# Performance work log

Hardware: AMD Instinct MI355X
Metric: run time of the kernel (lower is better)

The kernel has to match this reference:

```python
import jax, jax.numpy as jnp
import numpy as np

N, E = 50000, 800000
INF, ONF, HNF = 64, 64, 128
EPS = 1e-8


def qmul(p, q):
    # roma XYZW Hamilton product
    px, py, pz, pw = p[:, 0], p[:, 1], p[:, 2], p[:, 3]
    qx, qy, qz, qw = q[:, 0], q[:, 1], q[:, 2], q[:, 3]
    return jnp.stack([
        pw * qx + px * qw + py * qz - pz * qy,
        pw * qy - px * qz + py * qw + pz * qx,
        pw * qz + px * qy - py * qx + pz * qw,
        pw * qw - px * qx - py * qy - pz * qz,
    ], axis=1)


def qinv(q):
    conj = jnp.concatenate([-q[:, :3], q[:, 3:]], axis=1)
    return conj / jnp.sum(q * q, axis=1, keepdims=True)


def rot_apply(q, v):
    # rotate v by unit quaternion q (XYZW)
    qv, w = q[:, :3], q[:, 3:4]
    t = 2.0 * jnp.cross(qv, v)
    return v + w * t + jnp.cross(qv, t)


def quat_exponential(im):
    r = jnp.linalg.norm(im, axis=1, keepdims=True)
    u = im / r
    return jnp.concatenate([u * jnp.sin(r), jnp.cos(r)], axis=1)


def seg_sum(data, ids, n):
    return jax.ops.segment_sum(data, ids, num_segments=n)


def seg_mean(data, ids, n):
    s = seg_sum(data, ids, n)
    c = seg_sum(jnp.ones_like(data), ids, n)
    return s / jnp.maximum(c, 1.0)


def setup_inputs() -> dict:
    key = jax.random.key(0)
    ks = jax.random.split(key, 24)
    h = jax.random.normal(ks[0], (N, INF), jnp.float32)
    coord = jax.random.normal(ks[1], (N, 3), jnp.float32)
    q = jax.random.normal(ks[2], (N, 4), jnp.float32)
    quat = q / jnp.linalg.norm(q, axis=1, keepdims=True)
    edge_index = jax.random.randint(ks[3], (2, E), 0, N)

    def lin(k, fi, fo, scale=None):
        s = (1.0 / np.sqrt(fi)) if scale is None else scale
        return jax.random.uniform(k, (fi, fo), jnp.float32, -s, s)

    ein = 2 * INF + 8  # source, target, radial(1), quat_prod(4), unit_vecs(3)
    params = dict(
        We1=lin(ks[4], ein, HNF), be1=jnp.zeros((HNF,), jnp.float32),
        We2=lin(ks[5], HNF, HNF), be2=jnp.zeros((HNF,), jnp.float32),
        Wn1=lin(ks[6], HNF + INF, HNF), bn1=jnp.zeros((HNF,), jnp.float32),
        Wn2=lin(ks[7], HNF, ONF), bn2=jnp.zeros((ONF,), jnp.float32),
        Wc1=lin(ks[8], HNF, HNF), bc1=jnp.zeros((HNF,), jnp.float32),
        wc2=lin(ks[9], HNF, 1, scale=0.001),  # xavier gain 0.001, no bias
        Wq1=lin(ks[10], HNF, HNF), bq1=jnp.zeros((HNF,), jnp.float32),
        Wq2=lin(ks[11], HNF, 3), bq2=jnp.zeros((3,), jnp.float32),
    )
    return dict(h=h, edge_index=edge_index, coord=coord, quat=quat, **params)


def reference(h, edge_index, coord, quat,
              We1, be1, We2, be2, Wn1, bn1, Wn2, bn2,
              Wc1, bc1, wc2, Wq1, bq1, Wq2, bq2):
    silu = jax.nn.silu
    row, col = edge_index[0], edge_index[1]

    # invariants
    coord_diff = coord[row] - coord[col]                       # [E,3]
    qi = qinv(quat)
    quat_prod = qmul(qi[row], quat[col])                       # [E,4]
    radial = jnp.sum(coord_diff ** 2, axis=1, keepdims=True)   # [E,1]
    norm = jnp.sqrt(radial) + EPS
    unit_vecs = -rot_apply(qi[row], coord_diff / norm)         # [E,3]

    # edge model
    ein = jnp.concatenate([h[row], h[col], radial, quat_prod, unit_vecs], axis=1)
    edge_feat = silu(silu(ein @ We1 + be1) @ We2 + be2)        # [E,HNF]

    # coord model (mean agg)
    trans = coord_diff * (silu(edge_feat @ Wc1 + bc1) @ wc2)   # [E,3]
    coord = coord + seg_mean(trans, row, N)

    # quat model (mean agg)
    tan_vecs = silu(edge_feat @ Wq1 + bq1) @ Wq2 + bq2         # [E,3]
    rots = quat_exponential(seg_mean(tan_vecs, row, N))
    quat = qmul(quat, rots)

    # node model (sum agg), residual
    agg = seg_sum(edge_feat, row, N)
    nin = jnp.concatenate([h, agg], axis=1)
    h = h + (silu(nin @ Wn1 + bn1) @ Wn2 + bn2)
    return (h, coord, quat)
```

## Files before the change

### kernel.cpp

```cpp
#include <hip/hip_runtime.h>
#include <hip/hip_bf16.h>
#include <math.h>


#define N_NODES 50000
#define N_EDGES 800000
#define ASTR 172
#define NSTR 204

typedef __attribute__((ext_vector_type(4))) float f32x4;
typedef __attribute__((ext_vector_type(8))) short bf16x8;
typedef __attribute__((ext_vector_type(4))) unsigned short u16x4;
typedef __attribute__((ext_vector_type(8))) unsigned short u16x8;

static __device__ __forceinline__ unsigned short f2bf(float f) {
  return __builtin_bit_cast(unsigned short, __float2bfloat16(f));
}
static __device__ __forceinline__ float bf2f(unsigned short s) {
  unsigned int u = ((unsigned int)s) << 16;
  return __builtin_bit_cast(float, u);
}
static __device__ __forceinline__ float silu_f(float x) {
  return x * __builtin_amdgcn_rcpf(1.0f + __expf(-x));
}
static __device__ __forceinline__ void atomic_pk_add_bf16(unsigned int* addr,
                                                          float lo, float hi) {
  const unsigned int pk = ((unsigned int)f2bf(hi) << 16) | (unsigned int)f2bf(lo);
  asm volatile("global_atomic_pk_add_bf16 %0, %1, off"
               :: "v"((unsigned long long)(uintptr_t)addr), "v"(pk)
               : "memory");
}

static __device__ __forceinline__ void swz_do(const float* __restrict__ src,
                                              unsigned short* __restrict__ dst,
                                              int K, int NOUT, int NCT, int idx) {
  int lane = idx & 63, blk = idx >> 6;
  int ct = blk % NCT, kt = blk / NCT;
  int col = ct * 16 + (lane & 15);
  int kb = kt * 32 + (lane >> 4) * 8;
  u16x8 o;
  #pragma unroll
  for (int j = 0; j < 8; ++j) {
    int k = kb + j;
    o[j] = (k < K) ? f2bf(src[(size_t)k * NOUT + col]) : (unsigned short)0;
  }
  *(u16x8*)(dst + (size_t)idx * 8) = o;
}

__global__ __launch_bounds__(256) void prep1_kernel(
    const float* __restrict__ We1, const float* __restrict__ We2,
    const float* __restrict__ Wc1, const float* __restrict__ Wq1,
    const float* __restrict__ Wn1, const float* __restrict__ Wn2,
    const float* __restrict__ h,
    unsigned short* __restrict__ We1b, unsigned short* __restrict__ We2b,
    unsigned short* __restrict__ Wc1b, unsigned short* __restrict__ Wq1b,
    unsigned short* __restrict__ Wn1b, unsigned short* __restrict__ Wn2b,
    unsigned short* __restrict__ hb, uint4* __restrict__ zbase,
    const int* __restrict__ ei, int* __restrict__ cursor)
{
  const int b = blockIdx.x, t = threadIdx.x;
  if (b < 50) {
    if (b < 10)       swz_do(We1, We1b, 136, 128, 8, b*256 + t);
    else if (b < 18)  swz_do(We2, We2b, 128, 128, 8, (b-10)*256 + t);
    else if (b < 26)  swz_do(Wc1, Wc1b, 128, 128, 8, (b-18)*256 + t);
    else if (b < 34)  swz_do(Wq1, Wq1b, 128, 128, 8, (b-26)*256 + t);
    else if (b < 46) { int i = (b-34)*256 + t; if (i < 3072) swz_do(Wn1, Wn1b, 192, 128, 8, i); }
    else              swz_do(Wn2, Wn2b, 128, 64, 4, (b-46)*256 + t);
    return;
  }
  if (b < 832) {
    const int i16 = (b - 50) * 4096 + t * 16;
    if (i16 < N_NODES * 64) {
      u16x8 o0, o1;
      #pragma unroll
      for (int half = 0; half < 2; ++half) {
        f32x4 v0 = *(const f32x4*)(h + i16 + half*8);
        f32x4 v1 = *(const f32x4*)(h + i16 + half*8 + 4);
        #pragma unroll
        for (int i = 0; i < 4; ++i) {
          if (half == 0) { o0[i] = f2bf(v0[i]); o0[i+4] = f2bf(v1[i]); }
          else           { o1[i] = f2bf(v0[i]); o1[i+4] = f2bf(v1[i]); }
        }
      }
      *(u16x8*)(hb + i16) = o0;
      *(u16x8*)(hb + i16 + 8) = o1;
    }
    return;
  }
  if (b < 1687) {
    const int i = (b - 832) * 256 + t;
    if (i < 218750) {
      uint4 z; z.x = z.y = z.z = z.w = 0u;
      const int base = i * 4;
      zbase[base+0] = z; zbase[base+1] = z; zbase[base+2] = z; zbase[base+3] = z;
    }
    return;
  }
  const int e = (b - 1687) * 256 + t;
  if (e < N_EDGES) atomicAdd(&cursor[ei[e]], 1);
}

__global__ void scan_kernel(int* __restrict__ cursor) {
  __shared__ int s[1024];
  const int t = threadIdx.x;
  const int C = 49;
  const int base = t * C;
  int sum = 0;
  for (int i = 0; i < C; ++i) {
    int n = base + i;
    if (n < N_NODES) sum += cursor[n];
  }
  s[t] = sum;
  __syncthreads();
  for (int d = 1; d < 1024; d <<= 1) {
    int v = (t >= d) ? s[t - d] : 0;
    __syncthreads();
    s[t] += v;
    __syncthreads();
  }
  int run = s[t] - sum;
  for (int i = 0; i < C; ++i) {
    int n = base + i;
    if (n < N_NODES) {
      int d = cursor[n];
      cursor[n] = run;
      run += d;
    }
  }
}

__global__ void scatter_kernel(const int* __restrict__ ei, int* __restrict__ cursor,
                               int2* __restrict__ rc2) {
  int e = blockIdx.x * blockDim.x + threadIdx.x;
  if (e < N_EDGES) {
    int r = ei[e];
    int pos = atomicAdd(&cursor[r], 1);
    int2 v; v.x = r; v.y = ei[N_EDGES + e];
    rc2[pos] = v;
  }
}

template <int KT, int NCT>
static __device__ __forceinline__ void mmW2(const unsigned short* __restrict__ a0,
                                            const unsigned short* __restrict__ a1,
                                            int lk,
                                            const unsigned short* __restrict__ Wb,
                                            const float* __restrict__ bias,
                                            int lane, f32x4* acc0, f32x4* acc1) {
  #pragma unroll
  for (int ct = 0; ct < NCT; ++ct) {
    const f32x4 b = *(const f32x4*)&bias[ct*16 + lk*4];
    acc0[ct] = b; acc1[ct] = b;
  }
  __builtin_amdgcn_s_setprio(1);
  #pragma unroll
  for (int kt = 0; kt < KT; ++kt) {
    bf16x8 x0 = *(const bf16x8*)(a0 + kt*32 + lk*8);
    bf16x8 x1 = *(const bf16x8*)(a1 + kt*32 + lk*8);
    const u16x8* bb = (const u16x8*)Wb + (size_t)(kt*NCT)*64 + lane;
    #pragma unroll
    for (int ct = 0; ct < NCT; ++ct) {
      bf16x8 w = *(const bf16x8*)(bb + (size_t)ct*64);
      acc0[ct] = __builtin_amdgcn_mfma_f32_16x16x32_bf16(w, x0, acc0[ct], 0, 0, 0);
      acc1[ct] = __builtin_amdgcn_mfma_f32_16x16x32_bf16(w, x1, acc1[ct], 0, 0, 0);
    }
  }
  __builtin_amdgcn_s_setprio(0);
}

__global__ __launch_bounds__(128, 3) void edge_kernel(
    const unsigned short* __restrict__ hb,
    const float* __restrict__ coord, const float* __restrict__ quat,
    const int2* __restrict__ rc2,
    const unsigned short* __restrict__ We1b, const unsigned short* __restrict__ We2b,
    const unsigned short* __restrict__ Wc1b, const unsigned short* __restrict__ Wq1b,
    const float* __restrict__ be1, const float* __restrict__ be2,
    const float* __restrict__ bc1, const float* __restrict__ wc2,
    const float* __restrict__ bq1, const float* __restrict__ Wq2,
    const float* __restrict__ bq2,
    unsigned int* __restrict__ agg32, float* __restrict__ transS,
    float* __restrict__ tanS)
{
  __shared__ __align__(16) unsigned short AF[64 * ASTR];

  const int tid = threadIdx.x;
  const int wv = tid >> 6, lane = tid & 63;
  const int lr = lane & 15, lk = lane >> 4;
  const int row0 = wv*32 + lr, row1 = row0 + 16;

  const int xcd = blockIdx.x & 7, idx = blockIdx.x >> 3;
  const int q = 1562, rem = 4;
  const int bid = (xcd < rem ? xcd*(q+1) : rem*(q+1) + (xcd-rem)*q) + idx;
  const int e0 = bid * 64;

  const int2 p0v = rc2[e0 + row0];
  const int2 p1v = rc2[e0 + row1];
  const int r0 = p0v.x, c0 = p0v.y, r1 = p1v.x, c1 = p1v.y;

  {
    const unsigned short* hs0 = hb + (size_t)(lk < 2 ? r0 : c0) * 64 + (lk & 1) * 32;
    const unsigned short* hs1 = hb + (size_t)(lk < 2 ? r1 : c1) * 64 + (lk & 1) * 32;
    const int cb = lk * 32;
    #pragma unroll
    for (int j = 0; j < 32; j += 4) {
      *(u16x4*)&AF[row0*ASTR + cb + j] = *(const u16x4*)(hs0 + j);
      *(u16x4*)&AF[row1*ASTR + cb + j] = *(const u16x4*)(hs1 + j);
    }
  }
  const float cdx0 = coord[r0*3+0] - coord[c0*3+0];
  const float cdy0 = coord[r0*3+1] - coord[c0*3+1];
  const float cdz0 = coord[r0*3+2] - coord[c0*3+2];
  const float cdx1 = coord[r1*3+0] - coord[c1*3+0];
  const float cdy1 = coord[r1*3+1] - coord[c1*3+1];
  const float cdz1 = coord[r1*3+2] - coord[c1*3+2];
  if (lk < 2) {
    const int gr = lk ? r1 : r0, gc = lk ? c1 : c0, grow = lk ? row1 : row0;
    const float gx = lk ? cdx1 : cdx0, gy = lk ? cdy1 : cdy0, gz = lk ? cdz1 : cdz0;
    const float radial = gx*gx + gy*gy + gz*gz;
    const float nrm = sqrtf(radial) + 1e-8f;
    const f32x4 qr4 = *(const f32x4*)&quat[gr*4];
    const f32x4 qc4 = *(const f32x4*)&quat[gc*4];
    const float qix = -qr4[0], qiy = -qr4[1], qiz = -qr4[2], qiw = qr4[3];
    const float qcx = qc4[0], qcy = qc4[1], qcz = qc4[2], qcw = qc4[3];
    const float qpx = qiw*qcx + qix*qcw + qiy*qcz - qiz*qcy;
    const float qpy = qiw*qcy - qix*qcz + qiy*qcw + qiz*qcx;
    const float qpz = qiw*qcz + qix*qcy - qiy*qcx + qiz*qcw;
    const float qpw = qiw*qcw - qix*qcx - qiy*qcy - qiz*qcz;
    const float rinv = __builtin_amdgcn_rcpf(nrm);
    const float vx = gx*rinv, vy = gy*rinv, vz = gz*rinv;
    const float tx = 2.f*(qiy*vz - qiz*vy);
    const float ty = 2.f*(qiz*vx - qix*vz);
    const float tz = 2.f*(qix*vy - qiy*vx);
    const float ux = -(vx + qiw*tx + (qiy*tz - qiz*ty));
    const float uy = -(vy + qiw*ty + (qiz*tx - qix*tz));
    const float uz = -(vz + qiw*tz + (qix*ty - qiy*tx));
    u16x4 f0, f1;
    f0[0] = f2bf(radial); f0[1] = f2bf(qpx); f0[2] = f2bf(qpy); f0[3] = f2bf(qpz);
    f1[0] = f2bf(qpw);    f1[1] = f2bf(ux);  f1[2] = f2bf(uy);  f1[3] = f2bf(uz);
    *(u16x4*)&AF[grow*ASTR + 128] = f0;
    *(u16x4*)&AF[grow*ASTR + 132] = f1;
    const u16x4 z4 = {0, 0, 0, 0};
    #pragma unroll
    for (int j = 136; j < 160; j += 4) *(u16x4*)&AF[grow*ASTR + j] = z4;
  }

  f32x4 acc0[8], acc1[8];

  mmW2<5,8>(AF + row0*ASTR, AF + row1*ASTR, lk, We1b, be1, lane, acc0, acc1);
  #pragma unroll
  for (int ct = 0; ct < 8; ++ct) {
    const int ocb = ct*16 + lk*4;
    u16x4 k0, k1;
    #pragma unroll
    for (int i = 0; i < 4; ++i) {
      k0[i] = f2bf(silu_f(acc0[ct][i]));
      k1[i] = f2bf(silu_f(acc1[ct][i]));
    }
    *(u16x4*)&AF[row0*ASTR + ocb] = k0;
    *(u16x4*)&AF[row1*ASTR + ocb] = k1;
  }

  mmW2<4,8>(AF + row0*ASTR, AF + row1*ASTR, lk, We2b, be2, lane, acc0, acc1);
  #pragma unroll
  for (int ct = 0; ct < 8; ++ct) {
    const int ocb = ct*16 + lk*4;
    u16x4 k0, k1;
    #pragma unroll
    for (int i = 0; i < 4; ++i) {
      k0[i] = f2bf(silu_f(acc0[ct][i]));
      k1[i] = f2bf(silu_f(acc1[ct][i]));
    }
    *(u16x4*)&AF[row0*ASTR + ocb] = k0;
    *(u16x4*)&AF[row1*ASTR + ocb] = k1;
  }

  float pcs0 = 0.f, pcs1 = 0.f;
  mmW2<4,8>(AF + row0*ASTR, AF + row1*ASTR, lk, Wc1b, bc1, lane, acc0, acc1);
  #pragma unroll
  for (int ct = 0; ct < 8; ++ct) {
    const f32x4 w4 = *(const f32x4*)&wc2[ct*16 + lk*4];
    #pragma unroll
    for (int i = 0; i < 4; ++i) {
      pcs0 += silu_f(acc0[ct][i]) * w4[i];
      pcs1 += silu_f(acc1[ct][i]) * w4[i];
    }
  }
  pcs0 += __shfl_xor(pcs0, 16);  pcs0 += __shfl_xor(pcs0, 32);
  pcs1 += __shfl_xor(pcs1, 16);  pcs1 += __shfl_xor(pcs1, 32);

  float p00 = 0.f, p10 = 0.f, p20 = 0.f;
  float p01 = 0.f, p11 = 0.f, p21 = 0.f;
  mmW2<4,8>(AF + row0*ASTR, AF + row1*ASTR, lk, Wq1b, bq1, lane, acc0, acc1);
  #pragma unroll
  for (int ct = 0; ct < 8; ++ct) {
    const float* wq = &Wq2[(ct*16 + lk*4)*3];
    const f32x4 qa = *(const f32x4*)(wq);
    const f32x4 qb = *(const f32x4*)(wq + 4);
    const f32x4 qc = *(const f32x4*)(wq + 8);
    {
      const float v0 = silu_f(acc0[ct][0]);
      const float v1 = silu_f(acc0[ct][1]);
      const float v2 = silu_f(acc0[ct][2]);
      const float v3 = silu_f(acc0[ct][3]);
      p00 += v0*qa[0] + v1*qa[3] + v2*qb[2] + v3*qc[1];
      p10 += v0*qa[1] + v1*qb[0] + v2*qb[3] + v3*qc[2];
      p20 += v0*qa[2] + v1*qb[1] + v2*qc[0] + v3*qc[3];
    }
    {
      const float v0 = silu_f(acc1[ct][0]);
      const float v1 = silu_f(acc1[ct][1]);
      const float v2 = silu_f(acc1[ct][2]);
      const float v3 = silu_f(acc1[ct][3]);
      p01 += v0*qa[0] + v1*qa[3] + v2*qb[2] + v3*qc[1];
      p11 += v0*qa[1] + v1*qb[0] + v2*qb[3] + v3*qc[2];
      p21 += v0*qa[2] + v1*qb[1] + v2*qc[0] + v3*qc[3];
    }
  }
  p00 += __shfl_xor(p00, 16);  p00 += __shfl_xor(p00, 32);
  p10 += __shfl_xor(p10, 16);  p10 += __shfl_xor(p10, 32);
  p20 += __shfl_xor(p20, 16);  p20 += __shfl_xor(p20, 32);
  p01 += __shfl_xor(p01, 16);  p01 += __shfl_xor(p01, 32);
  p11 += __shfl_xor(p11, 16);  p11 += __shfl_xor(p11, 32);
  p21 += __shfl_xor(p21, 16);  p21 += __shfl_xor(p21, 32);

  if (lk < 3) {
    #pragma unroll
    for (int g = 0; g < 2; ++g) {
      const int rg = g ? r1 : r0;
      const int rUp = __shfl_up(rg, 1, 16);
      const int rDn = __shfl_down(rg, 1, 16);
      const bool head = (lr == 0) || (rUp != rg);
      const bool tail = (lr == 15) || (rDn != rg);
      const float cdj = (lk == 0) ? (g ? cdx1 : cdx0)
                      : (lk == 1) ? (g ? cdy1 : cdy0) : (g ? cdz1 : cdz0);
      const float pj  = (lk == 0) ? (g ? p01 : p00)
                      : (lk == 1) ? (g ? p11 : p10) : (g ? p21 : p20);
      float v1 = cdj * (g ? pcs1 : pcs0);
      float v2 = pj + bq2[lk];
      int f = head ? 1 : 0;
      #pragma unroll
      for (int d = 1; d < 16; d <<= 1) {
        const float o1 = __shfl_up(v1, d, 16);
        const float o2 = __shfl_up(v2, d, 16);
        const int   of = __shfl_up(f,  d, 16);
        if (lr >= d) {
          if (!f) { v1 += o1; v2 += o2; }
          f |= of;
        }
      }
      if (tail) {
        atomicAdd(&transS[rg*3 + lk], v1);
        atomicAdd(&tanS[rg*3 + lk], v2);
      }
    }
  }

  {
    float rl_ = 0.f, rh_ = 0.f;
    int prev = __builtin_amdgcn_readlane(r0, 0);
    #pragma unroll
    for (int k2 = 0; k2 < 32; ++k2) {
      const int rr = (k2 < 16) ? __builtin_amdgcn_readlane(r0, k2)
                               : __builtin_amdgcn_readlane(r1, k2 - 16);
      if (rr != prev) {
        atomic_pk_add_bf16(&agg32[(size_t)prev*64 + lane], rl_, rh_);
        rl_ = 0.f; rh_ = 0.f; prev = rr;
      }
      const unsigned int u = *(const unsigned int*)&AF[(wv*32 + k2)*ASTR + 2*lane];
      rl_ += bf2f((unsigned short)(u & 0xffffu));
      rh_ += bf2f((unsigned short)(u >> 16));
    }
    atomic_pk_add_bf16(&agg32[(size_t)prev*64 + lane], rl_, rh_);
  }
}

__global__ __launch_bounds__(256, 4) void node_kernel(
    const float* __restrict__ h, const unsigned short* __restrict__ hb,
    const float* __restrict__ coord, const float* __restrict__ quat,
    const unsigned short* __restrict__ aggb, const float* __restrict__ transS,
    const float* __restrict__ tanS, const int* __restrict__ cursor,
    const unsigned short* __restrict__ Wn1b, const unsigned short* __restrict__ Wn2b,
    const float* __restrict__ bn1, const float* __restrict__ bn2,
    float* __restrict__ out_h, float* __restrict__ out_c, float* __restrict__ out_q)
{
  __shared__ unsigned short A_[64][NSTR];
  const int tid = threadIdx.x;
  const int n0 = blockIdx.x * 64;

  {
    const int row = tid >> 2, sub = tid & 3;
    const int n = n0 + row;
    if (n < N_NODES) {
      if (sub < 2) {
        const unsigned short* hp = hb + (size_t)n*64 + sub*32;
        #pragma unroll
        for (int j = 0; j < 32; j += 4)
          *(u16x4*)&A_[row][sub*32 + j] = *(const u16x4*)(hp + j);
      } else {
        const unsigned short* ap = aggb + (size_t)n*128 + (sub - 2)*64;
        #pragma unroll
        for (int j = 0; j < 64; j += 8)
          *(u16x8*)&A_[row][64 + (sub - 2)*64 + j] = *(const u16x8*)(ap + j);
      }
    } else {
      const u16x4 z4 = {0, 0, 0, 0};
      if (sub < 2) {
        #pragma unroll
        for (int j = 0; j < 32; j += 4) *(u16x4*)&A_[row][sub*32 + j] = z4;
      } else {
        #pragma unroll
        for (int j = 0; j < 64; j += 4) *(u16x4*)&A_[row][64 + (sub - 2)*64 + j] = z4;
      }
    }
  }
  __syncthreads();

  const int wv = tid >> 6, lane = tid & 63;
  const int lr = lane & 15, lk = lane >> 4;
  const int nrow = wv*16 + lr;
  f32x4 acc[8];

  {
    #pragma unroll
    for (int ct = 0; ct < 8; ++ct)
      acc[ct] = *(const f32x4*)&bn1[ct*16 + lk*4];
    #pragma unroll
    for (int kt = 0; kt < 6; ++kt) {
      bf16x8 act = *(const bf16x8*)&A_[nrow][kt*32 + lk*8];
      const u16x8* bb = (const u16x8*)Wn1b + (size_t)(kt*8)*64 + lane;
      #pragma unroll
      for (int ct = 0; ct < 8; ++ct) {
        bf16x8 w = *(const bf16x8*)(bb + (size_t)ct*64);
        acc[ct] = __builtin_amdgcn_mfma_f32_16x16x32_bf16(w, act, acc[ct], 0, 0, 0);
      }
    }
  }
  #pragma unroll
  for (int ct = 0; ct < 8; ++ct) {
    const int ocb = ct*16 + lk*4;
    u16x4 pk;
    #pragma unroll
    for (int i = 0; i < 4; ++i) pk[i] = f2bf(silu_f(acc[ct][i]));
    *(u16x4*)&A_[nrow][ocb] = pk;
  }

  f32x4 acc2[4];
  {
    #pragma unroll
    for (int ct = 0; ct < 4; ++ct)
      acc2[ct] = *(const f32x4*)&bn2[ct*16 + lk*4];
    #pragma unroll
    for (int kt = 0; kt < 4; ++kt) {
      bf16x8 act = *(const bf16x8*)&A_[nrow][kt*32 + lk*8];
      const u16x8* bb = (const u16x8*)Wn2b + (size_t)(kt*4)*64 + lane;
      #pragma unroll
      for (int ct = 0; ct < 4; ++ct) {
        bf16x8 w = *(const bf16x8*)(bb + (size_t)ct*64);
        acc2[ct] = __builtin_amdgcn_mfma_f32_16x16x32_bf16(w, act, acc2[ct], 0, 0, 0);
      }
    }
  }
  const int n = n0 + nrow;
  if (n < N_NODES) {
    #pragma unroll
    for (int ct = 0; ct < 4; ++ct) {
      const int ocb = ct*16 + lk*4;
      const f32x4 h4 = *(const f32x4*)&h[(size_t)n*64 + ocb];
      f32x4 o;
      #pragma unroll
      for (int i = 0; i < 4; ++i) o[i] = h4[i] + acc2[ct][i];
      *(f32x4*)&out_h[(size_t)n*64 + ocb] = o;
    }
  }

  if (tid < 64) {
    const int nn = n0 + tid;
    if (nn < N_NODES) {
      const int deg = cursor[nn] - (nn ? cursor[nn-1] : 0);
      const float inv = 1.0f / fmaxf((float)deg, 1.0f);
      out_c[nn*3+0] = coord[nn*3+0] + transS[nn*3+0]*inv;
      out_c[nn*3+1] = coord[nn*3+1] + transS[nn*3+1]*inv;
      out_c[nn*3+2] = coord[nn*3+2] + transS[nn*3+2]*inv;
      const float ix = tanS[nn*3+0]*inv, iy = tanS[nn*3+1]*inv, iz = tanS[nn*3+2]*inv;
      const float rr = sqrtf(ix*ix + iy*iy + iz*iz);
      const float s = sinf(rr) / rr;
      const float rx = ix*s, ry = iy*s, rz = iz*s, rw = cosf(rr);
      const float px = quat[nn*4+0], py = quat[nn*4+1], pz = quat[nn*4+2], pw = quat[nn*4+3];
      out_q[nn*4+0] = pw*rx + px*rw + py*rz - pz*ry;
      out_q[nn*4+1] = pw*ry - px*rz + py*rw + pz*rx;
      out_q[nn*4+2] = pw*rz + px*ry - py*rx + pz*rw;
      out_q[nn*4+3] = pw*rw - px*rx - py*ry - pz*rz;
    }
  }
}

extern "C" void kernel_launch(void* const* d_in, const int* in_sizes, int n_in,
                              void* d_out, int out_size, void* d_ws, size_t ws_size,
                              hipStream_t stream) {
  (void)in_sizes; (void)n_in; (void)out_size; (void)ws_size;
  const float* h     = (const float*)d_in[0];
  const int*   ei    = (const int*)d_in[1];
  const float* coord = (const float*)d_in[2];
  const float* quat  = (const float*)d_in[3];
  const float* We1 = (const float*)d_in[4];  const float* be1 = (const float*)d_in[5];
  const float* We2 = (const float*)d_in[6];  const float* be2 = (const float*)d_in[7];
  const float* Wn1 = (const float*)d_in[8];  const float* bn1 = (const float*)d_in[9];
  const float* Wn2 = (const float*)d_in[10]; const float* bn2 = (const float*)d_in[11];
  const float* Wc1 = (const float*)d_in[12]; const float* bc1 = (const float*)d_in[13];
  const float* wc2 = (const float*)d_in[14];
  const float* Wq1 = (const float*)d_in[15]; const float* bq1 = (const float*)d_in[16];
  const float* Wq2 = (const float*)d_in[17]; const float* bq2 = (const float*)d_in[18];

  char* ws = (char*)d_ws;
  unsigned int* agg32  = (unsigned int*)(ws);
  unsigned short* aggb = (unsigned short*)(ws);
  float* transS = (float*)(ws + 12800000);
  float* tanS   = (float*)(ws + 13400000);
  int*   cursor = (int*)  (ws + 14200000);
  int2*  rc2    = (int2*) (ws + 14600064);
  unsigned short* We1b = (unsigned short*)(ws + 21000064);
  unsigned short* We2b = We1b + 5*8*64*8;
  unsigned short* Wc1b = We2b + 4*8*64*8;
  unsigned short* Wq1b = Wc1b + 4*8*64*8;
  unsigned short* Wn1b = Wq1b + 4*8*64*8;
  unsigned short* Wn2b = Wn1b + 6*8*64*8;
  unsigned short* hb   = (unsigned short*)(ws + 21204864);

  hipMemsetAsync(cursor, 0, 200000, stream);
  prep1_kernel<<<4812, 256, 0, stream>>>(
      We1, We2, Wc1, Wq1, Wn1, Wn2, h,
      We1b, We2b, Wc1b, Wq1b, Wn1b, Wn2b, hb, (uint4*)ws, ei, cursor);
  scan_kernel<<<1, 1024, 0, stream>>>(cursor);
  scatter_kernel<<<(N_EDGES + 255)/256, 256, 0, stream>>>(ei, cursor, rc2);

  edge_kernel<<<N_EDGES/64, 128, 0, stream>>>(
      hb, coord, quat, rc2, We1b, We2b, Wc1b, Wq1b,
      be1, be2, bc1, wc2, bq1, Wq2, bq2, agg32, transS, tanS);

  float* out_h = (float*)d_out;
  float* out_c = out_h + (size_t)N_NODES*64;
  float* out_q = out_c + (size_t)N_NODES*3;
  node_kernel<<<(N_NODES + 63)/64, 256, 0, stream>>>(
      h, hb, coord, quat, aggb, transS, tanS, cursor, Wn1b, Wn2b, bn1, bn2,
      out_h, out_c, out_q);
}
```

Baseline: 462.9 us.

## Fuse Wc1 and Wq1 GEMMs into one 256-column MFMA pass

After: 498.4 us. 7.7% more time.

```diff
diff --git a/kernel.cpp b/kernel.cpp
--- a/kernel.cpp
+++ b/kernel.cpp
@@ -31,9 +31,10 @@
                : "memory");
 }
 
-static __device__ __forceinline__ void swz_do(const float* __restrict__ src,
-                                              unsigned short* __restrict__ dst,
-                                              int K, int NOUT, int NCT, int idx) {
+static __device__ __forceinline__ void swz_do2(const float* __restrict__ src,
+                                               unsigned short* __restrict__ dst,
+                                               int K, int NOUT, int NCT,
+                                               int NCTDST, int CTOFF, int idx) {
   int lane = idx & 63, blk = idx >> 6;
   int ct = blk % NCT, kt = blk / NCT;
   int col = ct * 16 + (lane & 15);
@@ -44,7 +45,13 @@
     int k = kb + j;
     o[j] = (k < K) ? f2bf(src[(size_t)k * NOUT + col]) : (unsigned short)0;
   }
-  *(u16x8*)(dst + (size_t)idx * 8) = o;
+  const int dblk = kt * NCTDST + CTOFF + ct;
+  *(u16x8*)(dst + ((size_t)dblk * 64 + lane) * 8) = o;
+}
+static __device__ __forceinline__ void swz_do(const float* __restrict__ src,
+                                              unsigned short* __restrict__ dst,
+                                              int K, int NOUT, int NCT, int idx) {
+  swz_do2(src, dst, K, NOUT, NCT, NCT, 0, idx);
 }
 
 __global__ __launch_bounds__(256) void prep1_kernel(
@@ -53,7 +60,7 @@
     const float* __restrict__ Wn1, const float* __restrict__ Wn2,
     const float* __restrict__ h,
     unsigned short* __restrict__ We1b, unsigned short* __restrict__ We2b,
-    unsigned short* __restrict__ Wc1b, unsigned short* __restrict__ Wq1b,
+    unsigned short* __restrict__ Wcqb,
     unsigned short* __restrict__ Wn1b, unsigned short* __restrict__ Wn2b,
     unsigned short* __restrict__ hb, uint4* __restrict__ zbase,
     const int* __restrict__ ei, int* __restrict__ cursor)
@@ -62,8 +69,8 @@
   if (b < 50) {
     if (b < 10)       swz_do(We1, We1b, 136, 128, 8, b*256 + t);
     else if (b < 18)  swz_do(We2, We2b, 128, 128, 8, (b-10)*256 + t);
-    else if (b < 26)  swz_do(Wc1, Wc1b, 128, 128, 8, (b-18)*256 + t);
-    else if (b < 34)  swz_do(Wq1, Wq1b, 128, 128, 8, (b-26)*256 + t);
+    else if (b < 26)  swz_do2(Wc1, Wcqb, 128, 128, 8, 16, 0, (b-18)*256 + t);
+    else if (b < 34)  swz_do2(Wq1, Wcqb, 128, 128, 8, 16, 8, (b-26)*256 + t);
     else if (b < 46) { int i = (b-34)*256 + t; if (i < 3072) swz_do(Wn1, Wn1b, 192, 128, 8, i); }
     else              swz_do(Wn2, Wn2b, 128, 64, 4, (b-46)*256 + t);
     return;
@@ -168,12 +175,12 @@
   __builtin_amdgcn_s_setprio(0);
 }
 
-__global__ __launch_bounds__(128, 3) void edge_kernel(
+__global__ __launch_bounds__(128, 2) void edge_kernel(
     const unsigned short* __restrict__ hb,
     const float* __restrict__ coord, const float* __restrict__ quat,
     const int2* __restrict__ rc2,
     const unsigned short* __restrict__ We1b, const unsigned short* __restrict__ We2b,
-    const unsigned short* __restrict__ Wc1b, const unsigned short* __restrict__ Wq1b,
+    const unsigned short* __restrict__ Wcqb,
     const float* __restrict__ be1, const float* __restrict__ be2,
     const float* __restrict__ bc1, const float* __restrict__ wc2,
     const float* __restrict__ bq1, const float* __restrict__ Wq2,
@@ -274,48 +281,67 @@
     *(u16x4*)&AF[row1*ASTR + ocb] = k1;
   }
 
+  f32x4 accF0[16], accF1[16];
+  #pragma unroll
+  for (int ct = 0; ct < 16; ++ct) {
+    const f32x4 b = (ct < 8) ? *(const f32x4*)&bc1[ct*16 + lk*4]
+                             : *(const f32x4*)&bq1[(ct-8)*16 + lk*4];
+    accF0[ct] = b; accF1[ct] = b;
+  }
+  __builtin_amdgcn_s_setprio(1);
+  #pragma unroll
+  for (int kt = 0; kt < 4; ++kt) {
+    bf16x8 x0 = *(const bf16x8*)(AF + row0*ASTR + kt*32 + lk*8);
+    bf16x8 x1 = *(const bf16x8*)(AF + row1*ASTR + kt*32 + lk*8);
+    const u16x8* bb = (const u16x8*)Wcqb + (size_t)(kt*16)*64 + lane;
+    #pragma unroll
+    for (int ct = 0; ct < 16; ++ct) {
+      bf16x8 w = *(const bf16x8*)(bb + (size_t)ct*64);
+      accF0[ct] = __builtin_amdgcn_mfma_f32_16x16x32_bf16(w, x0, accF0[ct], 0, 0, 0);
+      accF1[ct] = __builtin_amdgcn_mfma_f32_16x16x32_bf16(w, x1, accF1[ct], 0, 0, 0);
+    }
+  }
+  __builtin_amdgcn_s_setprio(0);
+
   float pcs0 = 0.f, pcs1 = 0.f;
-  mmW2<4,8>(AF + row0*ASTR, AF + row1*ASTR, lk, Wc1b, bc1, lane, acc0, acc1);
+  float p00 = 0.f, p10 = 0.f, p20 = 0.f;
+  float p01 = 0.f, p11 = 0.f, p21 = 0.f;
   #pragma unroll
   for (int ct = 0; ct < 8; ++ct) {
     const f32x4 w4 = *(const f32x4*)&wc2[ct*16 + lk*4];
     #pragma unroll
     for (int i = 0; i < 4; ++i) {
-      pcs0 += silu_f(acc0[ct][i]) * w4[i];
-      pcs1 += silu_f(acc1[ct][i]) * w4[i];
-    }
-  }
-  pcs0 += __shfl_xor(pcs0, 16);  pcs0 += __shfl_xor(pcs0, 32);
-  pcs1 += __shfl_xor(pcs1, 16);  pcs1 += __shfl_xor(pcs1, 32);
-
-  float p00 = 0.f, p10 = 0.f, p20 = 0.f;
-  float p01 = 0.f, p11 = 0.f, p21 = 0.f;
-  mmW2<4,8>(AF + row0*ASTR, AF + row1*ASTR, lk, Wq1b, bq1, lane, acc0, acc1);
-  #pragma unroll
-  for (int ct = 0; ct < 8; ++ct) {
-    const float* wq = &Wq2[(ct*16 + lk*4)*3];
+      pcs0 += silu_f(accF0[ct][i]) * w4[i];
+      pcs1 += silu_f(accF1[ct][i]) * w4[i];
+    }
+  }
+  #pragma unroll
+  for (int ct = 8; ct < 16; ++ct) {
+    const float* wq = &Wq2[((ct-8)*16 + lk*4)*3];
     const f32x4 qa = *(const f32x4*)(wq);
     const f32x4 qb = *(const f32x4*)(wq + 4);
     const f32x4 qc = *(const f32x4*)(wq + 8);
     {
-      const float v0 = silu_f(acc0[ct][0]);
-      const float v1 = silu_f(acc0[ct][1]);
-      const float v2 = silu_f(acc0[ct][2]);
-      const float v3 = silu_f(acc0[ct][3]);
+      const float v0 = silu_f(accF0[ct][0]);
+      const float v1 = silu_f(accF0[ct][1]);
+      const float v2 = silu_f(accF0[ct][2]);
+      const float v3 = silu_f(accF0[ct][3]);
       p00 += v0*qa[0] + v1*qa[3] + v2*qb[2] + v3*qc[1];
       p10 += v0*qa[1] + v1*qb[0] + v2*qb[3] + v3*qc[2];
       p20 += v0*qa[2] + v1*qb[1] + v2*qc[0] + v3*qc[3];
     }
     {
-      const float v0 = silu_f(acc1[ct][0]);
-      const float v1 = silu_f(acc1[ct][1]);
-      const float v2 = silu_f(acc1[ct][2]);
-      const float v3 = silu_f(acc1[ct][3]);
+      const float v0 = silu_f(accF1[ct][0]);
+      const float v1 = silu_f(accF1[ct][1]);
+      const float v2 = silu_f(accF1[ct][2]);
+      const float v3 = silu_f(accF1[ct][3]);
       p01 += v0*qa[0] + v1*qa[3] + v2*qb[2] + v3*qc[1];
       p11 += v0*qa[1] + v1*qb[0] + v2*qb[3] + v3*qc[2];
       p21 += v0*qa[2] + v1*qb[1] + v2*qc[0] + v3*qc[3];
     }
   }
+  pcs0 += __shfl_xor(pcs0, 16);  pcs0 += __shfl_xor(pcs0, 32);
+  pcs1 += __shfl_xor(pcs1, 16);  pcs1 += __shfl_xor(pcs1, 32);
   p00 += __shfl_xor(p00, 16);  p00 += __shfl_xor(p00, 32);
   p10 += __shfl_xor(p10, 16);  p10 += __shfl_xor(p10, 32);
   p20 += __shfl_xor(p20, 16);  p20 += __shfl_xor(p20, 32);
@@ -520,21 +546,20 @@
   int2*  rc2    = (int2*) (ws + 14600064);
   unsigned short* We1b = (unsigned short*)(ws + 21000064);
   unsigned short* We2b = We1b + 5*8*64*8;
-  unsigned short* Wc1b = We2b + 4*8*64*8;
-  unsigned short* Wq1b = Wc1b + 4*8*64*8;
-  unsigned short* Wn1b = Wq1b + 4*8*64*8;
+  unsigned short* Wcqb = We2b + 4*8*64*8;
+  unsigned short* Wn1b = Wcqb + 4*16*64*8;
   unsigned short* Wn2b = Wn1b + 6*8*64*8;
   unsigned short* hb   = (unsigned short*)(ws + 21204864);
 
   hipMemsetAsync(cursor, 0, 200000, stream);
   prep1_kernel<<<4812, 256, 0, stream>>>(
       We1, We2, Wc1, Wq1, Wn1, Wn2, h,
-      We1b, We2b, Wc1b, Wq1b, Wn1b, Wn2b, hb, (uint4*)ws, ei, cursor);
+      We1b, We2b, Wcqb, Wn1b, Wn2b, hb, (uint4*)ws, ei, cursor);
   scan_kernel<<<1, 1024, 0, stream>>>(cursor);
   scatter_kernel<<<(N_EDGES + 255)/256, 256, 0, stream>>>(ei, cursor, rc2);
 
   edge_kernel<<<N_EDGES/64, 128, 0, stream>>>(
-      hb, coord, quat, rc2, We1b, We2b, Wc1b, Wq1b,
+      hb, coord, quat, rc2, We1b, We2b, Wcqb,
       be1, be2, bc1, wc2, bq1, Wq2, bq2, agg32, transS, tanS);
 
   float* out_h = (float*)d_out;
```
